# Kernel tuning notes

Hardware: AMD Instinct MI355X
Metric: run time of the kernel (lower is better)

The kernel has to match this reference:

```python
import jax, jax.numpy as jnp
import numpy as np

N = 8192
IN_F = 512
OUT_F = 512
N_SUB = 8


def setup_inputs() -> dict:
    key = jax.random.key(0)
    k1, k2, k3, k4 = jax.random.split(key, 4)
    input_features = jax.random.normal(k1, (N, IN_F), dtype=jnp.float32)
    # dense adjacency with small positive entries (normalized-adj-like)
    adj = jax.random.uniform(k2, (N, N), dtype=jnp.float32) / N
    subspace_labels = jax.random.randint(k3, (N,), 0, N_SUB, dtype=jnp.int32)
    # kaiming-uniform-style init per subspace weight
    bound = float(np.sqrt(6.0 / IN_F))
    W = jax.random.uniform(k4, (N_SUB, IN_F, OUT_F), dtype=jnp.float32,
                           minval=-bound, maxval=bound)
    return {"input_features": input_features, "adj": adj,
            "subspace_labels": subspace_labels, "W": W}


def reference(input_features, adj, subspace_labels, W):
    # Original: for each subspace s,
    #   output[mask_s] = adj[mask_s][:, mask_s] @ (X[mask_s] @ W[s])
    # Equivalently: per-node support uses that node's subspace weight, and
    # adjacency is masked to same-subspace pairs.
    n_sub = W.shape[0]
    support = jnp.zeros((input_features.shape[0], W.shape[2]),
                        dtype=input_features.dtype)
    for s in range(n_sub):  # small fixed loop over subspaces
        sel = (subspace_labels == s)[:, None]
        support = support + jnp.where(sel, input_features @ W[s], 0.0)
    # mask adjacency to intra-subspace edges: [N, N]
    same = (subspace_labels[:, None] == subspace_labels[None, :])
    masked_adj = jnp.where(same, adj, 0.0)
    return masked_adj @ support
```

## Files before the change

kernel.cpp:

```cpp
#include <hip/hip_runtime.h>
#include <hip/hip_bf16.h>

#define NN   8192
#define FF   512
#define NS   8
#define CAP  1152
#define KKT  (NS * CAP)

typedef __bf16 bf16x8 __attribute__((ext_vector_type(8)));
typedef float  f32x4  __attribute__((ext_vector_type(4)));

#define GLOAD_LDS(src, dst)                                                    \
    __builtin_amdgcn_global_load_lds(                                          \
        (const __attribute__((address_space(1))) void*)(src),                  \
        (__attribute__((address_space(3))) void*)(dst), 16, 0, 0)

__device__ __forceinline__ bf16x8 ldswz(const __bf16* lds, int row, int c) {
    return *(const bf16x8*)((const char*)lds + row * 128 + ((c ^ (row & 7)) << 4));
}

__global__ void bucket_kernel(const int* __restrict__ labels,
                              int* __restrict__ permP,
                              int* __restrict__ kk_of,
                              int* __restrict__ cnt) {
    int i = blockIdx.x * 256 + threadIdx.x;
    int s = labels[i];
    int p = atomicAdd(&cnt[s], 1);
    if (p < CAP) {
        int pos = s * CAP + p;
        permP[pos] = i;
        kk_of[i] = pos;
    } else {
        kk_of[i] = -1;
    }
}

__global__ void wt_kernel(const float* __restrict__ W, __bf16* __restrict__ WT) {
    __shared__ float tile[32][33];
    int s  = blockIdx.z;
    int n0 = blockIdx.x * 32, k0 = blockIdx.y * 32;
    int tx = threadIdx.x, ty = threadIdx.y;
    const float* Ws = W + (size_t)s * FF * FF;
    for (int r = 0; r < 4; ++r) {
        int k = k0 + ty + r * 8;
        tile[ty + r * 8][tx] = Ws[(size_t)k * FF + n0 + tx];
    }
    __syncthreads();
    __bf16* WTs = WT + (size_t)s * FF * FF;
    for (int r = 0; r < 4; ++r) {
        int n = n0 + ty + r * 8;
        WTs[(size_t)n * FF + k0 + tx] = (__bf16)tile[tx][ty + r * 8];
    }
}

__global__ __launch_bounds__(256) void xp_kernel(const float* __restrict__ X,
                                                 const int* __restrict__ permP,
                                                 __bf16* __restrict__ Xp) {
    int kk = blockIdx.x * 2 + (threadIdx.x >> 7);
    int c  = threadIdx.x & 127;
    int node = permP[kk];
    __align__(8) __bf16 v[4];
    if (node >= 0) {
        float4 x = *(const float4*)(X + (size_t)node * FF + c * 4);
        v[0] = (__bf16)x.x; v[1] = (__bf16)x.y;
        v[2] = (__bf16)x.z; v[3] = (__bf16)x.w;
    } else {
        v[0] = v[1] = v[2] = v[3] = (__bf16)0.0f;
    }
    *(uint2*)(Xp + (size_t)kk * FF + c * 4) = *(uint2*)v;
}

__global__ __launch_bounds__(256) void support_kernel(
        const __bf16* __restrict__ Xp, const __bf16* __restrict__ WT,
        __bf16* __restrict__ supT) {
    __shared__ __align__(1024) __bf16 Alds[64 * 64];
    __shared__ __align__(1024) __bf16 Blds[128 * 64];
    const int t = threadIdx.x, lane = t & 63, w = t >> 6;
    const int seg = blockIdx.x & 7;
    const int wi  = blockIdx.x >> 3;
    const int m0 = seg * CAP + (wi >> 2) * 64;
    const int n0 = (wi & 3) * 128;
    const int wm = w & 1, wn = w >> 1, l15 = lane & 15, q = lane >> 4;
    const int trow = t >> 3;
    const int cswz = (t & 7) ^ (trow & 7);
    const __bf16* Abase = Xp + (size_t)m0 * FF;
    const __bf16* Bbase = WT + (size_t)seg * FF * FF + (size_t)n0 * FF;
    f32x4 acc[2][4] = {};
    for (int k0 = 0; k0 < FF; k0 += 64) {
        #pragma unroll
        for (int p = 0; p < 2; ++p) {
            int row = p * 32 + trow;
            GLOAD_LDS(Abase + (size_t)row * FF + k0 + cswz * 8, Alds + p * 2048 + w * 512);
        }
        #pragma unroll
        for (int p = 0; p < 4; ++p) {
            int row = p * 32 + trow;
            GLOAD_LDS(Bbase + (size_t)row * FF + k0 + cswz * 8, Blds + p * 2048 + w * 512);
        }
        __syncthreads();
        #pragma unroll
        for (int h = 0; h < 2; ++h) {
            bf16x8 a[2], b[4];
            #pragma unroll
            for (int mi = 0; mi < 2; ++mi) a[mi] = ldswz(Alds, wm * 32 + mi * 16 + l15, h * 4 + q);
            #pragma unroll
            for (int ni = 0; ni < 4; ++ni) b[ni] = ldswz(Blds, wn * 64 + ni * 16 + l15, h * 4 + q);
            #pragma unroll
            for (int mi = 0; mi < 2; ++mi)
                #pragma unroll
                for (int ni = 0; ni < 4; ++ni)
                    acc[mi][ni] = __builtin_amdgcn_mfma_f32_16x16x32_bf16(a[mi], b[ni], acc[mi][ni], 0, 0, 0);
        }
        __syncthreads();
    }
    #pragma unroll
    for (int mi = 0; mi < 2; ++mi) {
        int kk = m0 + wm * 32 + mi * 16 + q * 4;
        #pragma unroll
        for (int ni = 0; ni < 4; ++ni) {
            int n = n0 + wn * 64 + ni * 16 + l15;
            __align__(8) __bf16 v[4];
            #pragma unroll
            for (int r = 0; r < 4; ++r) v[r] = (__bf16)acc[mi][ni][r];
            *(uint2*)(supT + (size_t)n * KKT + kk) = *(uint2*)v;
        }
    }
}

__global__ __launch_bounds__(256) void compact_kernel(
        const float* __restrict__ adj, const int* __restrict__ permP,
        const int* __restrict__ kk_of, __bf16* __restrict__ adjc) {
    __shared__ __align__(16) __bf16 row[CAP];
    int t = threadIdx.x;
    int ii = blockIdx.x;
    for (int i = t; i < CAP * 2 / 4; i += 256) ((int*)row)[i] = 0;
    int node = permP[ii];
    __syncthreads();
    if (node >= 0) {
        int base = (ii / CAP) * CAP;
        const float4* arow = (const float4*)(adj + (size_t)node * NN);
        const int4*  kkrow = (const int4*)kk_of;
        #pragma unroll
        for (int p = 0; p < NN / (256 * 4); ++p) {
            int idx = p * 256 + t;
            float4 a = arow[idx];
            int4  kk = kkrow[idx];
            int j;
            j = kk.x - base; if ((unsigned)j < CAP) row[j] = (__bf16)a.x;
            j = kk.y - base; if ((unsigned)j < CAP) row[j] = (__bf16)a.y;
            j = kk.z - base; if ((unsigned)j < CAP) row[j] = (__bf16)a.z;
            j = kk.w - base; if ((unsigned)j < CAP) row[j] = (__bf16)a.w;
        }
    }
    __syncthreads();
    if (t < CAP * 2 / 16) {
        ((uint4*)(adjc + (size_t)ii * CAP))[t] = ((const uint4*)row)[t];
    }
}

__global__ __launch_bounds__(256) void gemm_kernel(
        const __bf16* __restrict__ adjc, const __bf16* __restrict__ supT,
        const int* __restrict__ permP, float* __restrict__ out) {
    __shared__ __align__(1024) __bf16 Alds[64 * 64];
    __shared__ __align__(1024) __bf16 Blds[128 * 64];
    const int t = threadIdx.x, lane = t & 63, w = t >> 6;
    const int seg = blockIdx.x & 7;
    const int wi  = blockIdx.x >> 3;
    const int m0 = seg * CAP + (wi >> 2) * 64;
    const int n0 = (wi & 3) * 128;
    const int segbase = seg * CAP;
    const int wm = w & 1, wn = w >> 1, l15 = lane & 15, q = lane >> 4;
    const int trow = t >> 3;
    const int cswz = (t & 7) ^ (trow & 7);
    const __bf16* Abase = adjc + (size_t)m0 * CAP;
    const __bf16* Bbase = supT + (size_t)n0 * KKT + segbase;
    f32x4 acc[2][4] = {};
    for (int j0 = 0; j0 < CAP; j0 += 64) {
        #pragma unroll
        for (int p = 0; p < 2; ++p) {
            int row = p * 32 + trow;
            GLOAD_LDS(Abase + (size_t)row * CAP + j0 + cswz * 8, Alds + p * 2048 + w * 512);
        }
        #pragma unroll
        for (int p = 0; p < 4; ++p) {
            int row = p * 32 + trow;
            GLOAD_LDS(Bbase + (size_t)row * KKT + j0 + cswz * 8, Blds + p * 2048 + w * 512);
        }
        __syncthreads();
        #pragma unroll
        for (int h = 0; h < 2; ++h) {
            bf16x8 a[2], b[4];
            #pragma unroll
            for (int mi = 0; mi < 2; ++mi) a[mi] = ldswz(Alds, wm * 32 + mi * 16 + l15, h * 4 + q);
            #pragma unroll
            for (int ni = 0; ni < 4; ++ni) b[ni] = ldswz(Blds, wn * 64 + ni * 16 + l15, h * 4 + q);
            #pragma unroll
            for (int mi = 0; mi < 2; ++mi)
                #pragma unroll
                for (int ni = 0; ni < 4; ++ni)
                    acc[mi][ni] = __builtin_amdgcn_mfma_f32_16x16x32_bf16(a[mi], b[ni], acc[mi][ni], 0, 0, 0);
        }
        __syncthreads();
    }
    const int colb = n0 + wn * 64 + l15;
    #pragma unroll
    for (int mi = 0; mi < 2; ++mi) {
        int rowb = m0 + wm * 32 + mi * 16 + q * 4;
        #pragma unroll
        for (int r = 0; r < 4; ++r) {
            int node = permP[rowb + r];
            if (node >= 0) {
                float* o = out + (size_t)node * FF + colb;
                #pragma unroll
                for (int ni = 0; ni < 4; ++ni) o[ni * 16] = acc[mi][ni][r];
            }
        }
    }
}

extern "C" void kernel_launch(void* const* d_in, const int* in_sizes, int n_in,
                              void* d_out, int out_size, void* d_ws, size_t ws_size,
                              hipStream_t stream) {
    const float* X      = (const float*)d_in[0];
    const float* adj    = (const float*)d_in[1];
    const int*   labels = (const int*)d_in[2];
    const float* W      = (const float*)d_in[3];
    float* out = (float*)d_out;

    char* ws = (char*)d_ws;
    int*    cnt   = (int*)ws;
    int*    kk_of = (int*)(ws + 1024);
    int*    permP = (int*)(ws + (64u << 10));
    __bf16* WT    = (__bf16*)(ws + (1u << 20));
    __bf16* Xp    = (__bf16*)(ws + (6u << 20));
    __bf16* supT  = (__bf16*)(ws + (16u << 20));
    __bf16* adjc  = (__bf16*)(ws + (26u << 20));

    hipMemsetAsync(cnt, 0, NS * sizeof(int), stream);
    hipMemsetAsync(permP, 0xFF, (size_t)KKT * sizeof(int), stream);
    bucket_kernel<<<NN / 256, 256, 0, stream>>>(labels, permP, kk_of, cnt);
    wt_kernel<<<dim3(16, 16, 8), dim3(32, 8), 0, stream>>>(W, WT);
    xp_kernel<<<KKT / 2, 256, 0, stream>>>(X, permP, Xp);
    support_kernel<<<576, 256, 0, stream>>>(Xp, WT, supT);
    compact_kernel<<<KKT, 256, 0, stream>>>(adj, permP, kk_of, adjc);
    gemm_kernel<<<576, 256, 0, stream>>>(adjc, supT, permP, out);
}
```

Measured before the change: 464.7 us.

## Double-buffer GEMM tiles, enlarge M tile, batch compaction rows, aggregate bucket atomics

Both GEMM kernels now use 128x128 tiles with double-buffered LDS, so the loads for the next K slice are issued while MFMAs run on the current one, and the grid drops from 576 to 288 blocks. The compact kernel handles four adjacency rows per block, reusing each kk_of load across those rows. The bucket kernel counts within the block in shared memory first and does one global atomic per subspace. The trade-offs are fewer blocks than the 256 CUs can evenly fill, higher register and LDS use per block, and the gather of adj still dominates memory traffic.

```diff
diff --git a/kernel.cpp b/kernel.cpp
--- a/kernel.cpp
+++ b/kernel.cpp
@@ -19,15 +19,35 @@
     return *(const bf16x8*)((const char*)lds + row * 128 + ((c ^ (row & 7)) << 4));
 }
 
+__device__ __forceinline__ void stage_tile(const __bf16* __restrict__ gsrc,
+                                           size_t stride, __bf16* lds,
+                                           int koff, int trow, int cswz, int w) {
+    #pragma unroll
+    for (int p = 0; p < 4; ++p) {
+        int row = p * 32 + trow;
+        GLOAD_LDS(gsrc + (size_t)row * stride + koff + cswz * 8,
+                  lds + p * 2048 + w * 512);
+    }
+}
+
 __global__ void bucket_kernel(const int* __restrict__ labels,
                               int* __restrict__ permP,
                               int* __restrict__ kk_of,
                               int* __restrict__ cnt) {
-    int i = blockIdx.x * 256 + threadIdx.x;
+    __shared__ int lcnt[NS];
+    __shared__ int lbase[NS];
+    int t = threadIdx.x;
+    if (t < NS) lcnt[t] = 0;
+    __syncthreads();
+    int i = blockIdx.x * 256 + t;
     int s = labels[i];
-    int p = atomicAdd(&cnt[s], 1);
-    if (p < CAP) {
-        int pos = s * CAP + p;
+    int p = atomicAdd(&lcnt[s], 1);
+    __syncthreads();
+    if (t < NS) lbase[t] = atomicAdd(&cnt[t], lcnt[t]);
+    __syncthreads();
+    int rank = lbase[s] + p;
+    if (rank < CAP) {
+        int pos = s * CAP + rank;
         permP[pos] = i;
         kk_of[i] = pos;
     } else {
@@ -73,49 +93,48 @@
 __global__ __launch_bounds__(256) void support_kernel(
         const __bf16* __restrict__ Xp, const __bf16* __restrict__ WT,
         __bf16* __restrict__ supT) {
-    __shared__ __align__(1024) __bf16 Alds[64 * 64];
-    __shared__ __align__(1024) __bf16 Blds[128 * 64];
+    __shared__ __align__(1024) __bf16 Alds[2][128 * 64];
+    __shared__ __align__(1024) __bf16 Blds[2][128 * 64];
     const int t = threadIdx.x, lane = t & 63, w = t >> 6;
     const int seg = blockIdx.x & 7;
     const int wi  = blockIdx.x >> 3;
-    const int m0 = seg * CAP + (wi >> 2) * 64;
+    const int m0 = seg * CAP + (wi >> 2) * 128;
     const int n0 = (wi & 3) * 128;
     const int wm = w & 1, wn = w >> 1, l15 = lane & 15, q = lane >> 4;
     const int trow = t >> 3;
     const int cswz = (t & 7) ^ (trow & 7);
     const __bf16* Abase = Xp + (size_t)m0 * FF;
     const __bf16* Bbase = WT + (size_t)seg * FF * FF + (size_t)n0 * FF;
-    f32x4 acc[2][4] = {};
-    for (int k0 = 0; k0 < FF; k0 += 64) {
-        #pragma unroll
-        for (int p = 0; p < 2; ++p) {
-            int row = p * 32 + trow;
-            GLOAD_LDS(Abase + (size_t)row * FF + k0 + cswz * 8, Alds + p * 2048 + w * 512);
-        }
-        #pragma unroll
-        for (int p = 0; p < 4; ++p) {
-            int row = p * 32 + trow;
-            GLOAD_LDS(Bbase + (size_t)row * FF + k0 + cswz * 8, Blds + p * 2048 + w * 512);
-        }
-        __syncthreads();
+    f32x4 acc[4][4] = {};
+    const int NT = FF / 64;
+    stage_tile(Abase, FF, Alds[0], 0, trow, cswz, w);
+    stage_tile(Bbase, FF, Blds[0], 0, trow, cswz, w);
+    __syncthreads();
+    int cur = 0;
+    for (int it = 0; it < NT; ++it) {
+        if (it + 1 < NT) {
+            stage_tile(Abase, FF, Alds[cur ^ 1], (it + 1) * 64, trow, cswz, w);
+            stage_tile(Bbase, FF, Blds[cur ^ 1], (it + 1) * 64, trow, cswz, w);
+        }
         #pragma unroll
         for (int h = 0; h < 2; ++h) {
-            bf16x8 a[2], b[4];
-            #pragma unroll
-            for (int mi = 0; mi < 2; ++mi) a[mi] = ldswz(Alds, wm * 32 + mi * 16 + l15, h * 4 + q);
-            #pragma unroll
-            for (int ni = 0; ni < 4; ++ni) b[ni] = ldswz(Blds, wn * 64 + ni * 16 + l15, h * 4 + q);
-            #pragma unroll
-            for (int mi = 0; mi < 2; ++mi)
+            bf16x8 a[4], b[4];
+            #pragma unroll
+            for (int mi = 0; mi < 4; ++mi) a[mi] = ldswz(Alds[cur], wm * 64 + mi * 16 + l15, h * 4 + q);
+            #pragma unroll
+            for (int ni = 0; ni < 4; ++ni) b[ni] = ldswz(Blds[cur], wn * 64 + ni * 16 + l15, h * 4 + q);
+            #pragma unroll
+            for (int mi = 0; mi < 4; ++mi)
                 #pragma unroll
                 for (int ni = 0; ni < 4; ++ni)
                     acc[mi][ni] = __builtin_amdgcn_mfma_f32_16x16x32_bf16(a[mi], b[ni], acc[mi][ni], 0, 0, 0);
         }
         __syncthreads();
-    }
-    #pragma unroll
-    for (int mi = 0; mi < 2; ++mi) {
-        int kk = m0 + wm * 32 + mi * 16 + q * 4;
+        cur ^= 1;
+    }
+    #pragma unroll
+    for (int mi = 0; mi < 4; ++mi) {
+        int kk = m0 + wm * 64 + mi * 16 + q * 4;
         #pragma unroll
         for (int ni = 0; ni < 4; ++ni) {
             int n = n0 + wn * 64 + ni * 16 + l15;
@@ -130,43 +149,46 @@
 __global__ __launch_bounds__(256) void compact_kernel(
         const float* __restrict__ adj, const int* __restrict__ permP,
         const int* __restrict__ kk_of, __bf16* __restrict__ adjc) {
-    __shared__ __align__(16) __bf16 row[CAP];
+    __shared__ __align__(16) __bf16 rows[4][CAP];
     int t = threadIdx.x;
-    int ii = blockIdx.x;
-    for (int i = t; i < CAP * 2 / 4; i += 256) ((int*)row)[i] = 0;
-    int node = permP[ii];
-    __syncthreads();
-    if (node >= 0) {
-        int base = (ii / CAP) * CAP;
-        const float4* arow = (const float4*)(adj + (size_t)node * NN);
-        const int4*  kkrow = (const int4*)kk_of;
-        #pragma unroll
-        for (int p = 0; p < NN / (256 * 4); ++p) {
-            int idx = p * 256 + t;
-            float4 a = arow[idx];
-            int4  kk = kkrow[idx];
-            int j;
-            j = kk.x - base; if ((unsigned)j < CAP) row[j] = (__bf16)a.x;
-            j = kk.y - base; if ((unsigned)j < CAP) row[j] = (__bf16)a.y;
-            j = kk.z - base; if ((unsigned)j < CAP) row[j] = (__bf16)a.z;
-            j = kk.w - base; if ((unsigned)j < CAP) row[j] = (__bf16)a.w;
-        }
-    }
-    __syncthreads();
-    if (t < CAP * 2 / 16) {
-        ((uint4*)(adjc + (size_t)ii * CAP))[t] = ((const uint4*)row)[t];
-    }
+    int ii0 = blockIdx.x * 4;
+    for (int i = t; i < 4 * CAP / 2; i += 256) ((int*)rows)[i] = 0;
+    int nd[4];
+    #pragma unroll
+    for (int r = 0; r < 4; ++r) nd[r] = permP[ii0 + r];
+    int base = (ii0 / CAP) * CAP;
+    __syncthreads();
+    const int4* kkrow = (const int4*)kk_of;
+    #pragma unroll
+    for (int p = 0; p < NN / (256 * 4); ++p) {
+        int idx = p * 256 + t;
+        int4 kk = kkrow[idx];
+        int jx = kk.x - base, jy = kk.y - base, jz = kk.z - base, jw = kk.w - base;
+        #pragma unroll
+        for (int r = 0; r < 4; ++r) {
+            if (nd[r] >= 0) {
+                float4 a = ((const float4*)(adj + (size_t)nd[r] * NN))[idx];
+                if ((unsigned)jx < CAP) rows[r][jx] = (__bf16)a.x;
+                if ((unsigned)jy < CAP) rows[r][jy] = (__bf16)a.y;
+                if ((unsigned)jz < CAP) rows[r][jz] = (__bf16)a.z;
+                if ((unsigned)jw < CAP) rows[r][jw] = (__bf16)a.w;
+            }
+        }
+    }
+    __syncthreads();
+    uint4* dst = (uint4*)(adjc + (size_t)ii0 * CAP);
+    for (int i = t; i < 576; i += 256) dst[i] = ((const uint4*)rows)[i];
 }
 
 __global__ __launch_bounds__(256) void gemm_kernel(
         const __bf16* __restrict__ adjc, const __bf16* __restrict__ supT,
         const int* __restrict__ permP, float* __restrict__ out) {
-    __shared__ __align__(1024) __bf16 Alds[64 * 64];
-    __shared__ __align__(1024) __bf16 Blds[128 * 64];
+    __shared__ __align__(1024) __bf16 Alds[2][128 * 64];
+    __shared__ __align__(1024) __bf16 Blds[2][128 * 64];
     const int t = threadIdx.x, lane = t & 63, w = t >> 6;
     const int seg = blockIdx.x & 7;
     const int wi  = blockIdx.x >> 3;
-    const int m0 = seg * CAP + (wi >> 2) * 64;
+    const int m0 = seg * CAP + (wi >> 2) * 128;
     const int n0 = (wi & 3) * 128;
     const int segbase = seg * CAP;
     const int wm = w & 1, wn = w >> 1, l15 = lane & 15, q = lane >> 4;
@@ -174,38 +196,37 @@
     const int cswz = (t & 7) ^ (trow & 7);
     const __bf16* Abase = adjc + (size_t)m0 * CAP;
     const __bf16* Bbase = supT + (size_t)n0 * KKT + segbase;
-    f32x4 acc[2][4] = {};
-    for (int j0 = 0; j0 < CAP; j0 += 64) {
-        #pragma unroll
-        for (int p = 0; p < 2; ++p) {
-            int row = p * 32 + trow;
-            GLOAD_LDS(Abase + (size_t)row * CAP + j0 + cswz * 8, Alds + p * 2048 + w * 512);
-        }
-        #pragma unroll
-        for (int p = 0; p < 4; ++p) {
-            int row = p * 32 + trow;
-            GLOAD_LDS(Bbase + (size_t)row * KKT + j0 + cswz * 8, Blds + p * 2048 + w * 512);
-        }
-        __syncthreads();
+    f32x4 acc[4][4] = {};
+    const int NT = CAP / 64;
+    stage_tile(Abase, CAP, Alds[0], 0, trow, cswz, w);
+    stage_tile(Bbase, KKT, Blds[0], 0, trow, cswz, w);
+    __syncthreads();
+    int cur = 0;
+    for (int it = 0; it < NT; ++it) {
+        if (it + 1 < NT) {
+            stage_tile(Abase, CAP, Alds[cur ^ 1], (it + 1) * 64, trow, cswz, w);
+            stage_tile(Bbase, KKT, Blds[cur ^ 1], (it + 1) * 64, trow, cswz, w);
+        }
         #pragma unroll
         for (int h = 0; h < 2; ++h) {
-            bf16x8 a[2], b[4];
-            #pragma unroll
-            for (int mi = 0; mi < 2; ++mi) a[mi] = ldswz(Alds, wm * 32 + mi * 16 + l15, h * 4 + q);
-            #pragma unroll
-            for (int ni = 0; ni < 4; ++ni) b[ni] = ldswz(Blds, wn * 64 + ni * 16 + l15, h * 4 + q);
-            #pragma unroll
-            for (int mi = 0; mi < 2; ++mi)
+            bf16x8 a[4], b[4];
+            #pragma unroll
+            for (int mi = 0; mi < 4; ++mi) a[mi] = ldswz(Alds[cur], wm * 64 + mi * 16 + l15, h * 4 + q);
+            #pragma unroll
+            for (int ni = 0; ni < 4; ++ni) b[ni] = ldswz(Blds[cur], wn * 64 + ni * 16 + l15, h * 4 + q);
+            #pragma unroll
+            for (int mi = 0; mi < 4; ++mi)
                 #pragma unroll
                 for (int ni = 0; ni < 4; ++ni)
                     acc[mi][ni] = __builtin_amdgcn_mfma_f32_16x16x32_bf16(a[mi], b[ni], acc[mi][ni], 0, 0, 0);
         }
         __syncthreads();
+        cur ^= 1;
     }
     const int colb = n0 + wn * 64 + l15;
     #pragma unroll
-    for (int mi = 0; mi < 2; ++mi) {
-        int rowb = m0 + wm * 32 + mi * 16 + q * 4;
+    for (int mi = 0; mi < 4; ++mi) {
+        int rowb = m0 + wm * 64 + mi * 16 + q * 4;
         #pragma unroll
         for (int r = 0; r < 4; ++r) {
             int node = permP[rowb + r];
@@ -241,7 +262,7 @@
     bucket_kernel<<<NN / 256, 256, 0, stream>>>(labels, permP, kk_of, cnt);
     wt_kernel<<<dim3(16, 16, 8), dim3(32, 8), 0, stream>>>(W, WT);
     xp_kernel<<<KKT / 2, 256, 0, stream>>>(X, permP, Xp);
-    support_kernel<<<576, 256, 0, stream>>>(Xp, WT, supT);
-    compact_kernel<<<KKT, 256, 0, stream>>>(adj, permP, kk_of, adjc);
-    gemm_kernel<<<576, 256, 0, stream>>>(adjc, supT, permP, out);
-}
+    support_kernel<<<288, 256, 0, stream>>>(Xp, WT, supT);
+    compact_kernel<<<KKT / 4, 256, 0, stream>>>(adj, permP, kk_of, adjc);
+    gemm_kernel<<<288, 256, 0, stream>>>(adjc, supT, permP, out);
+}
```

New measurement: 458.1 us. No clear change (-1.4%).
